# Optimization experiments

Hardware: AMD Instinct MI355X
Metric: run time of the kernel (lower is better)

The kernel has to match this reference:

```python
import jax, jax.numpy as jnp
import numpy as np


def feature_map(x):
    # phi(x) = elu(x) + 1 (ensures positivity)
    return jax.nn.elu(x) + 1.0


def setup_inputs() -> dict:
    key = jax.random.key(0)
    k0, k1, k2, k3 = jax.random.split(key, 4)
    B, T, d_model, D = 4, 4096, 1024, 128
    x = jax.random.normal(k0, (B, T, d_model), dtype=jnp.float32)
    s = 1.0 / np.sqrt(d_model)
    Wq = jax.random.normal(k1, (d_model, D), dtype=jnp.float32) * s
    Wk = jax.random.normal(k2, (d_model, D), dtype=jnp.float32) * s
    Wv = jax.random.normal(k3, (d_model, D), dtype=jnp.float32) * s
    return {"x": x, "Wq": Wq, "Wk": Wk, "Wv": Wv}


def _causal_linear_attention(phi_q, phi_k, v):
    # phi_q, phi_k: [B,T,D]; v: [B,T,Dv]
    B, T, D = phi_q.shape
    Dv = v.shape[-1]
    # time-major for scan: [T,B,D]
    qT = jnp.swapaxes(phi_q, 0, 1)
    kT = jnp.swapaxes(phi_k, 0, 1)
    vT = jnp.swapaxes(v, 0, 1)

    def step(carry, inp):
        kv, ks = carry                       # kv: [B,D,Dv], ks: [B,D]
        qt, kt, vt = inp                     # each [B,D] / [B,Dv]
        kv = kv + kt[:, :, None] * vt[:, None, :]   # k_t^T v_t outer product
        ks = ks + kt
        num = jnp.einsum('bd,bdv->bv', qt, kv)      # [B,Dv]
        den = jnp.einsum('bd,bd->b', qt, ks)[:, None]
        return (kv, ks), num / den

    init = (jnp.zeros((B, D, Dv), phi_q.dtype), jnp.zeros((B, D), phi_q.dtype))
    _, outT = jax.lax.scan(step, init, (qT, kT, vT))  # outT: [T,B,Dv]
    return jnp.swapaxes(outT, 0, 1)


def reference(x, Wq, Wk, Wv):
    q = x @ Wq
    k = x @ Wk
    v = x @ Wv
    phi_q = feature_map(q)
    phi_k = feature_map(k)
    # dropout is identity in eval mode
    return _causal_linear_attention(phi_q, phi_k, v)
```

## Files before the change

### kernel.cpp

```cpp
#include <hip/hip_runtime.h>

#define DMODEL 1024
#define DHEAD 128
#define CHUNK 128
#define NCHUNK 32

typedef __attribute__((ext_vector_type(4))) float f32x4;
typedef __attribute__((ext_vector_type(8))) short bf16x8;

__device__ __forceinline__ unsigned short f2bf(float f) {
  union { float f; unsigned u; } v; v.f = f;
  unsigned r = v.u + 0x7FFF + ((v.u >> 16) & 1);
  return (unsigned short)(r >> 16);
}
__device__ __forceinline__ float bf2f(unsigned short h) {
  union { unsigned u; float f; } v; v.u = ((unsigned)h) << 16;
  return v.f;
}
__device__ __forceinline__ unsigned cvtpk(float lo, float hi) {
  unsigned r;
  asm("v_cvt_pk_bf16_f32 %0, %1, %2" : "=v"(r) : "v"(lo), "v"(hi));
  return r;
}
__device__ __forceinline__ void gload16(const void* g, void* l) {
  __builtin_amdgcn_global_load_lds(
      (const __attribute__((address_space(1))) unsigned int*)g,
      (__attribute__((address_space(3))) unsigned int*)l, 16, 0, 0);
}

__global__ __launch_bounds__(256) void transpose_w_kernel(
    const float* __restrict__ Wq, const float* __restrict__ Wk,
    const float* __restrict__ Wv, unsigned short* __restrict__ WT) {
  int id = blockIdx.x * 256 + threadIdx.x;
  int w = id >> 17;
  int rem = id & 131071;
  int n = rem >> 10;
  int k = rem & 1023;
  const float* W = (w == 0) ? Wq : (w == 1) ? Wk : Wv;
  WT[id] = f2bf(W[(size_t)k * DHEAD + n]);
}

__global__ __launch_bounds__(256) void proj_kernel(
    const float* __restrict__ x, const unsigned short* __restrict__ WT,
    unsigned short* __restrict__ phiQ, unsigned short* __restrict__ phiK,
    unsigned short* __restrict__ Vb) {
  const int bid = blockIdx.x;
  const int xcd = bid & 7;
  const int slot = bid >> 3;
  const int n0 = (slot & 1) << 6;
  const int m0 = ((xcd << 6) | (slot >> 1)) << 5;

  __shared__ float xs[32][64];
  __shared__ unsigned short wl[3][64][64];

  const int tid = threadIdx.x;
  const int wave = tid >> 6;
  const int lane = tid & 63;
  const int lrow = lane & 15, kgrp = lane >> 4;

  f32x4 acc[3][2];
#pragma unroll
  for (int w3 = 0; w3 < 3; ++w3)
#pragma unroll
    for (int mi = 0; mi < 2; ++mi) acc[w3][mi] = (f32x4)0.0f;

  for (int kk = 0; kk < DMODEL; kk += 64) {
    if (kk) __syncthreads();
#pragma unroll
    for (int i = 0; i < 2; ++i) {
      int instr = i * 4 + wave;
      int row = instr * 4 + (lane >> 4);
      int slotc = lane & 15;
      int gcol = (slotc ^ (row & 7)) << 2;
      gload16(&x[(size_t)(m0 + row) * DMODEL + kk + gcol],
              (char*)xs + instr * 1024);
    }
#pragma unroll
    for (int i = 0; i < 6; ++i) {
      int j = i * 4 + wave;
      int w3 = j >> 3;
      int jj = j & 7;
      int row = jj * 8 + (lane >> 3);
      int slotc = lane & 7;
      int gcol = (slotc ^ (row & 7)) << 3;
      gload16(&WT[(size_t)w3 * (DHEAD * DMODEL) + (size_t)(n0 + row) * DMODEL + kk + gcol],
              (char*)wl + w3 * 8192 + jj * 1024);
    }
    __syncthreads();

#pragma unroll
    for (int ks2 = 0; ks2 < 2; ++ks2) {
      bf16x8 af[2];
#pragma unroll
      for (int mi = 0; mi < 2; ++mi) {
        int arow = mi * 16 + lrow;
        int s0 = ks2 * 8 + kgrp * 2;
        const float4 f0 = *reinterpret_cast<const float4*>(
            &xs[arow][(s0 ^ (arow & 7)) << 2]);
        const float4 f1 = *reinterpret_cast<const float4*>(
            &xs[arow][((s0 + 1) ^ (arow & 7)) << 2]);
        union { unsigned u[4]; bf16x8 v; } p;
        p.u[0] = cvtpk(f0.x, f0.y);
        p.u[1] = cvtpk(f0.z, f0.w);
        p.u[2] = cvtpk(f1.x, f1.y);
        p.u[3] = cvtpk(f1.z, f1.w);
        af[mi] = p.v;
      }
#pragma unroll
      for (int w3 = 0; w3 < 3; ++w3) {
        int brow = wave * 16 + lrow;
        int bs = ks2 * 4 + kgrp;
        bf16x8 bf = *reinterpret_cast<const bf16x8*>(
            &wl[w3][brow][(bs ^ (brow & 7)) << 3]);
#pragma unroll
        for (int mi = 0; mi < 2; ++mi)
          acc[w3][mi] = __builtin_amdgcn_mfma_f32_16x16x32_bf16(af[mi], bf, acc[w3][mi], 0, 0, 0);
      }
    }
  }
#pragma unroll
  for (int w3 = 0; w3 < 3; ++w3) {
    unsigned short* outp = (w3 == 0) ? phiQ : (w3 == 1) ? phiK : Vb;
#pragma unroll
    for (int mi = 0; mi < 2; ++mi)
#pragma unroll
      for (int r = 0; r < 4; ++r) {
        int row = m0 + mi * 16 + kgrp * 4 + r;
        int col = n0 + wave * 16 + lrow;
        float v = acc[w3][mi][r];
        if (w3 < 2) v = (v > 0.0f) ? (v + 1.0f) : __expf(v);
        outp[(size_t)row * DHEAD + col] = f2bf(v);
      }
  }
}

__global__ __launch_bounds__(256) void chunkkv_kernel(
    const unsigned short* __restrict__ phiK, const unsigned short* __restrict__ Vb,
    float* __restrict__ KVc, float* __restrict__ ksc) {
  const int c = blockIdx.x;
  const int yv = blockIdx.y;
  const size_t base = (size_t)c * CHUNK * DHEAD;
  __shared__ unsigned short kt[128][136];
  __shared__ unsigned short vt[64][136];
  __shared__ float csum[2][128];
  const int tid = threadIdx.x;
  const int wave = tid >> 6, lane = tid & 63;
  const int lrow = lane & 15, kgrp = lane >> 4;

  {
    int t = tid & 127, dp = tid >> 7;
#pragma unroll
    for (int i = 0; i < 8; ++i) {
      int d0 = (dp + 2 * i) * 8;
      uint4 k4 = *reinterpret_cast<const uint4*>(&phiK[base + (size_t)t * DHEAD + d0]);
      const unsigned short* kp = reinterpret_cast<const unsigned short*>(&k4);
#pragma unroll
      for (int j = 0; j < 8; ++j) kt[d0 + j][t] = kp[j];
    }
#pragma unroll
    for (int i = 0; i < 4; ++i) {
      int dl = (dp + 2 * i) * 8;
      uint4 v4 = *reinterpret_cast<const uint4*>(
          &Vb[base + (size_t)t * DHEAD + yv * 64 + dl]);
      const unsigned short* vp = reinterpret_cast<const unsigned short*>(&v4);
#pragma unroll
      for (int j = 0; j < 8; ++j) vt[dl + j][t] = vp[j];
    }
  }
  __syncthreads();

  f32x4 acc[8];
#pragma unroll
  for (int j = 0; j < 8; ++j) acc[j] = (f32x4)0.0f;
#pragma unroll
  for (int ks = 0; ks < 4; ++ks) {
    int t0 = ks * 32 + kgrp * 8;
    bf16x8 afrag = *reinterpret_cast<const bf16x8*>(&vt[wave * 16 + lrow][t0]);
#pragma unroll
    for (int tc = 0; tc < 8; ++tc) {
      bf16x8 bfrag = *reinterpret_cast<const bf16x8*>(&kt[tc * 16 + lrow][t0]);
      acc[tc] = __builtin_amdgcn_mfma_f32_16x16x32_bf16(afrag, bfrag, acc[tc], 0, 0, 0);
    }
  }
  float* KVout = KVc + (size_t)c * (DHEAD * DHEAD);
#pragma unroll
  for (int tc = 0; tc < 8; ++tc)
#pragma unroll
    for (int r = 0; r < 4; ++r) {
      int dv = yv * 64 + wave * 16 + kgrp * 4 + r;
      int d = tc * 16 + lrow;
      KVout[dv * DHEAD + d] = acc[tc][r];
    }
  if (yv == 0) {
    int d = tid & 127, hh = tid >> 7;
    float s = 0.0f;
    for (int t = hh * 64; t < hh * 64 + 64; ++t) s += bf2f(kt[d][t]);
    csum[hh][d] = s;
    __syncthreads();
    if (tid < 128) ksc[(size_t)c * DHEAD + tid] = csum[0][tid] + csum[1][tid];
  }
}

__global__ __launch_bounds__(256) void prefix_kernel(
    const float* __restrict__ KVc, const float* __restrict__ ksc,
    unsigned short* __restrict__ KVp, float* __restrict__ ksp) {
  if (blockIdx.x < 256) {
    int id = blockIdx.x * 256 + threadIdx.x;
    int b = id >> 14;
    int e = id & 16383;
    size_t base = (size_t)b * NCHUNK * 16384 + e;
    float acc = 0.0f;
    for (int c = 0; c < NCHUNK; ++c) {
      KVp[base + (size_t)c * 16384] = f2bf(acc);
      acc += KVc[base + (size_t)c * 16384];
    }
  } else {
    for (int i = threadIdx.x; i < 512; i += 256) {
      int b = i >> 7, d = i & 127;
      size_t base = (size_t)b * NCHUNK * DHEAD + d;
      float acc = 0.0f;
      for (int c = 0; c < NCHUNK; ++c) {
        ksp[base + (size_t)c * DHEAD] = acc;
        acc += ksc[base + (size_t)c * DHEAD];
      }
    }
  }
}

__global__ __launch_bounds__(256) void out_kernel(
    const unsigned short* __restrict__ phiQ, const unsigned short* __restrict__ phiK,
    const unsigned short* __restrict__ Vb, const unsigned short* __restrict__ KVp,
    const float* __restrict__ ksp, float* __restrict__ outp) {
  const int c = blockIdx.x;
  const int h = blockIdx.y;
  const size_t kvbase = (size_t)c * CHUNK * DHEAD;
  const size_t qbase = kvbase + (size_t)h * 64 * DHEAD;
  __shared__ unsigned short qb[64][136];
  __shared__ unsigned short kb[128][136];
  __shared__ unsigned short vt[128][136];
  __shared__ float dsum[4][64];
  __shared__ float ks_l[128];
  const int tid = threadIdx.x;
  const int wave = tid >> 6, lane = tid & 63;
  const int lrow = lane & 15, kgrp = lane >> 4;

#pragma unroll
  for (int it = 0; it < 4; ++it) {
    int idx = it * 256 + tid;
    int t = idx >> 4;
    int d0 = (idx & 15) << 3;
    *reinterpret_cast<uint4*>(&qb[t][d0]) =
        *reinterpret_cast<const uint4*>(&phiQ[qbase + (size_t)t * DHEAD + d0]);
  }
  if (tid < 128) ks_l[tid] = ksp[(size_t)c * DHEAD + tid];
  if (h == 0) {
#pragma unroll
    for (int it = 0; it < 4; ++it) {
      int idx = it * 256 + tid;
      int t = idx >> 4;
      int d0 = (idx & 15) << 3;
      *reinterpret_cast<uint4*>(&kb[t][d0]) =
          *reinterpret_cast<const uint4*>(&phiK[kvbase + (size_t)t * DHEAD + d0]);
    }
    int t = tid & 63, dp = tid >> 6;
#pragma unroll
    for (int i = 0; i < 4; ++i) {
      int d0 = (dp + 4 * i) * 8;
      uint4 v4 = *reinterpret_cast<const uint4*>(&Vb[kvbase + (size_t)t * DHEAD + d0]);
      const unsigned short* vp = reinterpret_cast<const unsigned short*>(&v4);
#pragma unroll
      for (int j = 0; j < 8; ++j) vt[d0 + j][t] = vp[j];
    }
  } else {
#pragma unroll
    for (int it = 0; it < 8; ++it) {
      int idx = it * 256 + tid;
      int t = idx >> 4;
      int d0 = (idx & 15) << 3;
      *reinterpret_cast<uint4*>(&kb[t][d0]) =
          *reinterpret_cast<const uint4*>(&phiK[kvbase + (size_t)t * DHEAD + d0]);
    }
    int t = tid & 127, dp = tid >> 7;
#pragma unroll
    for (int i = 0; i < 8; ++i) {
      int d0 = (dp + 2 * i) * 8;
      uint4 v4 = *reinterpret_cast<const uint4*>(&Vb[kvbase + (size_t)t * DHEAD + d0]);
      const unsigned short* vp = reinterpret_cast<const unsigned short*>(&v4);
#pragma unroll
      for (int j = 0; j < 8; ++j) vt[d0 + j][t] = vp[j];
    }
  }
  __syncthreads();

  if (h == 0) {
    f32x4 sa[4];
#pragma unroll
    for (int i = 0; i < 4; ++i) sa[i] = (f32x4)0.0f;
#pragma unroll
    for (int ks = 0; ks < 4; ++ks) {
      int d0 = ks * 32 + kgrp * 8;
      bf16x8 af = *reinterpret_cast<const bf16x8*>(&qb[wave * 16 + lrow][d0]);
#pragma unroll
      for (int tc = 0; tc < 4; ++tc) {
        bf16x8 bf = *reinterpret_cast<const bf16x8*>(&kb[tc * 16 + lrow][d0]);
        sa[tc] = __builtin_amdgcn_mfma_f32_16x16x32_bf16(af, bf, sa[tc], 0, 0, 0);
      }
    }
    __syncthreads();
#pragma unroll
    for (int tc = 0; tc < 4; ++tc)
#pragma unroll
      for (int r = 0; r < 4; ++r) {
        int trow = wave * 16 + kgrp * 4 + r;
        int s = tc * 16 + lrow;
        kb[trow][s] = f2bf((s <= trow) ? sa[tc][r] : 0.0f);
      }
  } else {
    f32x4 sa[8];
#pragma unroll
    for (int i = 0; i < 8; ++i) sa[i] = (f32x4)0.0f;
#pragma unroll
    for (int ks = 0; ks < 4; ++ks) {
      int d0 = ks * 32 + kgrp * 8;
      bf16x8 af = *reinterpret_cast<const bf16x8*>(&qb[wave * 16 + lrow][d0]);
#pragma unroll
      for (int tc = 0; tc < 8; ++tc) {
        bf16x8 bf = *reinterpret_cast<const bf16x8*>(&kb[tc * 16 + lrow][d0]);
        sa[tc] = __builtin_amdgcn_mfma_f32_16x16x32_bf16(af, bf, sa[tc], 0, 0, 0);
      }
    }
    __syncthreads();
#pragma unroll
    for (int tc = 0; tc < 8; ++tc)
#pragma unroll
      for (int r = 0; r < 4; ++r) {
        int trow = wave * 16 + kgrp * 4 + r;
        int s = tc * 16 + lrow;
        kb[trow][s] = f2bf((s <= 64 + trow) ? sa[tc][r] : 0.0f);
      }
  }
  __syncthreads();

  {
    int t = tid & 63, h4 = tid >> 6;
    float s = 0.0f;
    if (h4 < 2) {
      if (h4 == 0 || h == 1) {
        for (int j = h4 * 64; j < h4 * 64 + 64; ++j) s += bf2f(kb[t][j]);
      }
    } else {
      for (int j = (h4 - 2) * 64; j < (h4 - 2) * 64 + 64; ++j)
        s += bf2f(qb[t][j]) * ks_l[j];
    }
    dsum[h4][t] = s;
  }

  f32x4 acc[8];
#pragma unroll
  for (int i = 0; i < 8; ++i) acc[i] = (f32x4)0.0f;
  {
    const int nks = (h == 0) ? 2 : 4;
    for (int ks = 0; ks < nks; ++ks) {
      int t0 = ks * 32 + kgrp * 8;
      bf16x8 af = *reinterpret_cast<const bf16x8*>(&kb[wave * 16 + lrow][t0]);
#pragma unroll
      for (int tc = 0; tc < 8; ++tc) {
        bf16x8 bf = *reinterpret_cast<const bf16x8*>(&vt[tc * 16 + lrow][t0]);
        acc[tc] = __builtin_amdgcn_mfma_f32_16x16x32_bf16(af, bf, acc[tc], 0, 0, 0);
      }
    }
  }
  __syncthreads();

#pragma unroll
  for (int it = 0; it < 8; ++it) {
    int idx = it * 256 + tid;
    int dv = idx >> 4;
    int d0 = (idx & 15) << 3;
    *reinterpret_cast<uint4*>(&vt[dv][d0]) =
        *reinterpret_cast<const uint4*>(&KVp[(size_t)c * 16384 + (size_t)dv * DHEAD + d0]);
  }
  __syncthreads();

#pragma unroll
  for (int ks = 0; ks < 4; ++ks) {
    int d0 = ks * 32 + kgrp * 8;
    bf16x8 af = *reinterpret_cast<const bf16x8*>(&qb[wave * 16 + lrow][d0]);
#pragma unroll
    for (int tc = 0; tc < 8; ++tc) {
      bf16x8 bf = *reinterpret_cast<const bf16x8*>(&vt[tc * 16 + lrow][d0]);
      acc[tc] = __builtin_amdgcn_mfma_f32_16x16x32_bf16(af, bf, acc[tc], 0, 0, 0);
    }
  }

#pragma unroll
  for (int tc = 0; tc < 8; ++tc)
#pragma unroll
    for (int r = 0; r < 4; ++r) {
      int trow = wave * 16 + kgrp * 4 + r;
      int dv = tc * 16 + lrow;
      float den = dsum[0][trow] + dsum[1][trow] + dsum[2][trow] + dsum[3][trow];
      outp[qbase + (size_t)trow * DHEAD + dv] = acc[tc][r] / den;
    }
}

extern "C" void kernel_launch(void* const* d_in, const int* in_sizes, int n_in,
                              void* d_out, int out_size, void* d_ws, size_t ws_size,
                              hipStream_t stream) {
  const float* x  = (const float*)d_in[0];
  const float* Wq = (const float*)d_in[1];
  const float* Wk = (const float*)d_in[2];
  const float* Wv = (const float*)d_in[3];
  float* out = (float*)d_out;
  char* ws = (char*)d_ws;
  unsigned short* phiQ = (unsigned short*)(ws + 0);
  unsigned short* phiK = (unsigned short*)(ws + 4194304);
  unsigned short* Vb   = (unsigned short*)(ws + 8388608);
  unsigned short* WT   = (unsigned short*)(ws + 12582912);
  float*          KVc  = (float*)(ws + 13369344);
  unsigned short* KVp  = (unsigned short*)(ws + 21757952);
  float*          ksc  = (float*)(ws + 25952256);
  float*          ksp  = (float*)(ws + 26017792);

  transpose_w_kernel<<<1536, 256, 0, stream>>>(Wq, Wk, Wv, WT);
  proj_kernel<<<1024, 256, 0, stream>>>(x, WT, phiQ, phiK, Vb);
  chunkkv_kernel<<<dim3(128, 2), 256, 0, stream>>>(phiK, Vb, KVc, ksc);
  prefix_kernel<<<257, 256, 0, stream>>>(KVc, ksc, KVp, ksp);
  out_kernel<<<dim3(128, 2), 256, 0, stream>>>(phiQ, phiK, Vb, KVp, ksp, out);
}
```

Baseline: 55.55 us.

## Split projection kernel per weight matrix with 64x64 output tiles

The fused Q/K/V projection kernel, where each 256-thread block computed a 32x64 tile for all three weights, becomes a 128-thread kernel on a 256x6 grid. Each block now handles one weight matrix and a 64-row by 64-column tile, so each wave owns 32 rows and does 2x4 MFMAs per k-step. The aim is higher arithmetic intensity per block and more independent blocks. The cost is that each x tile is now fetched by six blocks instead of two, and the XCD-aware block swizzle is dropped. That could raise global and L2 traffic on the large fp32 input.

```diff
diff --git a/kernel.cpp b/kernel.cpp
--- a/kernel.cpp
+++ b/kernel.cpp
@@ -40,51 +40,50 @@
   WT[id] = f2bf(W[(size_t)k * DHEAD + n]);
 }
 
-__global__ __launch_bounds__(256) void proj_kernel(
+__global__ __launch_bounds__(128) void proj_kernel(
     const float* __restrict__ x, const unsigned short* __restrict__ WT,
     unsigned short* __restrict__ phiQ, unsigned short* __restrict__ phiK,
     unsigned short* __restrict__ Vb) {
-  const int bid = blockIdx.x;
-  const int xcd = bid & 7;
-  const int slot = bid >> 3;
-  const int n0 = (slot & 1) << 6;
-  const int m0 = ((xcd << 6) | (slot >> 1)) << 5;
-
-  __shared__ float xs[32][64];
-  __shared__ unsigned short wl[3][64][64];
+  const int which = blockIdx.y >> 1;
+  const int nh = blockIdx.y & 1;
+  const int n0 = nh << 6;
+  const unsigned short* Wt = WT + (size_t)which * (DHEAD * DMODEL);
+  unsigned short* outp = (which == 0) ? phiQ : (which == 1) ? phiK : Vb;
+  const int m0 = blockIdx.x * 64;
+
+  __shared__ float xs[64][64];
+  __shared__ unsigned short ws[64][64];
 
   const int tid = threadIdx.x;
   const int wave = tid >> 6;
   const int lane = tid & 63;
   const int lrow = lane & 15, kgrp = lane >> 4;
 
-  f32x4 acc[3][2];
-#pragma unroll
-  for (int w3 = 0; w3 < 3; ++w3)
-#pragma unroll
-    for (int mi = 0; mi < 2; ++mi) acc[w3][mi] = (f32x4)0.0f;
+  f32x4 acc[2][4];
+#pragma unroll
+  for (int i = 0; i < 2; ++i)
+#pragma unroll
+    for (int j = 0; j < 4; ++j) acc[i][j] = (f32x4)0.0f;
 
   for (int kk = 0; kk < DMODEL; kk += 64) {
     if (kk) __syncthreads();
 #pragma unroll
-    for (int i = 0; i < 2; ++i) {
-      int instr = i * 4 + wave;
+    for (int i = 0; i < 8; ++i) {
+      int instr = i * 2 + wave;
       int row = instr * 4 + (lane >> 4);
-      int slotc = lane & 15;
-      int gcol = (slotc ^ (row & 7)) << 2;
+      int slot = lane & 15;
+      int gcol = (slot ^ (row & 7)) << 2;
       gload16(&x[(size_t)(m0 + row) * DMODEL + kk + gcol],
               (char*)xs + instr * 1024);
     }
 #pragma unroll
-    for (int i = 0; i < 6; ++i) {
-      int j = i * 4 + wave;
-      int w3 = j >> 3;
-      int jj = j & 7;
-      int row = jj * 8 + (lane >> 3);
-      int slotc = lane & 7;
-      int gcol = (slotc ^ (row & 7)) << 3;
-      gload16(&WT[(size_t)w3 * (DHEAD * DMODEL) + (size_t)(n0 + row) * DMODEL + kk + gcol],
-              (char*)wl + w3 * 8192 + jj * 1024);
+    for (int i = 0; i < 4; ++i) {
+      int instr = i * 2 + wave;
+      int row = instr * 8 + (lane >> 3);
+      int slot = lane & 7;
+      int gcol = (slot ^ (row & 7)) << 3;
+      gload16(&Wt[(size_t)(n0 + row) * DMODEL + kk + gcol],
+              (char*)ws + instr * 1024);
     }
     __syncthreads();
 
@@ -92,8 +91,8 @@
     for (int ks2 = 0; ks2 < 2; ++ks2) {
       bf16x8 af[2];
 #pragma unroll
-      for (int mi = 0; mi < 2; ++mi) {
-        int arow = mi * 16 + lrow;
+      for (int mr = 0; mr < 2; ++mr) {
+        int arow = wave * 32 + mr * 16 + lrow;
         int s0 = ks2 * 8 + kgrp * 2;
         const float4 f0 = *reinterpret_cast<const float4*>(
             &xs[arow][(s0 ^ (arow & 7)) << 2]);
@@ -104,34 +103,31 @@
         p.u[1] = cvtpk(f0.z, f0.w);
         p.u[2] = cvtpk(f1.x, f1.y);
         p.u[3] = cvtpk(f1.z, f1.w);
-        af[mi] = p.v;
-      }
-#pragma unroll
-      for (int w3 = 0; w3 < 3; ++w3) {
-        int brow = wave * 16 + lrow;
+        af[mr] = p.v;
+      }
+#pragma unroll
+      for (int nt = 0; nt < 4; ++nt) {
+        int brow = nt * 16 + lrow;
         int bs = ks2 * 4 + kgrp;
         bf16x8 bf = *reinterpret_cast<const bf16x8*>(
-            &wl[w3][brow][(bs ^ (brow & 7)) << 3]);
-#pragma unroll
-        for (int mi = 0; mi < 2; ++mi)
-          acc[w3][mi] = __builtin_amdgcn_mfma_f32_16x16x32_bf16(af[mi], bf, acc[w3][mi], 0, 0, 0);
-      }
-    }
-  }
-#pragma unroll
-  for (int w3 = 0; w3 < 3; ++w3) {
-    unsigned short* outp = (w3 == 0) ? phiQ : (w3 == 1) ? phiK : Vb;
-#pragma unroll
-    for (int mi = 0; mi < 2; ++mi)
+            &ws[brow][(bs ^ (brow & 7)) << 3]);
+        acc[0][nt] = __builtin_amdgcn_mfma_f32_16x16x32_bf16(af[0], bf, acc[0][nt], 0, 0, 0);
+        acc[1][nt] = __builtin_amdgcn_mfma_f32_16x16x32_bf16(af[1], bf, acc[1][nt], 0, 0, 0);
+      }
+    }
+  }
+#pragma unroll
+  for (int mr = 0; mr < 2; ++mr)
+#pragma unroll
+    for (int nt = 0; nt < 4; ++nt)
 #pragma unroll
       for (int r = 0; r < 4; ++r) {
-        int row = m0 + mi * 16 + kgrp * 4 + r;
-        int col = n0 + wave * 16 + lrow;
-        float v = acc[w3][mi][r];
-        if (w3 < 2) v = (v > 0.0f) ? (v + 1.0f) : __expf(v);
+        int row = m0 + wave * 32 + mr * 16 + kgrp * 4 + r;
+        int col = n0 + nt * 16 + lrow;
+        float v = acc[mr][nt][r];
+        if (which < 2) v = (v > 0.0f) ? (v + 1.0f) : __expf(v);
         outp[(size_t)row * DHEAD + col] = f2bf(v);
       }
-  }
 }
 
 __global__ __launch_bounds__(256) void chunkkv_kernel(
@@ -423,7 +419,7 @@
   float*          ksp  = (float*)(ws + 26017792);
 
   transpose_w_kernel<<<1536, 256, 0, stream>>>(Wq, Wk, Wv, WT);
-  proj_kernel<<<1024, 256, 0, stream>>>(x, WT, phiQ, phiK, Vb);
+  proj_kernel<<<dim3(256, 6), 128, 0, stream>>>(x, WT, phiQ, phiK, Vb);
   chunkkv_kernel<<<dim3(128, 2), 256, 0, stream>>>(phiK, Vb, KVc, ksc);
   prefix_kernel<<<257, 256, 0, stream>>>(KVc, ksc, KVp, ksp);
   out_kernel<<<dim3(128, 2), 256, 0, stream>>>(phiQ, phiK, Vb, KVp, ksp, out);
```

After: 60.11 us. +8.2%, slower.
